# Optimization experiments

Measured on AMD Instinct MI355X. Metric: run time of the kernel, lower is better.

Reference implementation:

```python
import jax, jax.numpy as jnp
import numpy as np

B, P, EPG = 1000, 100, 1200  # graphs, nodes/graph, edges/graph
IN, HID, OUT, K = 16, 64, 5, 3


def setup_inputs() -> dict:
    key = jax.random.key(0)
    ks = jax.random.split(key, 12)
    offs = jnp.repeat(jnp.arange(B, dtype=jnp.int32) * P, EPG)
    src = jax.random.randint(ks[0], (B * EPG,), 0, P, dtype=jnp.int32) + offs
    dst = jax.random.randint(ks[1], (B * EPG,), 0, P, dtype=jnp.int32) + offs
    graph_ids = jnp.repeat(jnp.arange(B, dtype=jnp.int32), P)
    feat = jax.random.normal(ks[2], (B * P, IN), dtype=jnp.float32)

    def lin(k1, fan_in, fan_out):
        s = 1.0 / np.sqrt(fan_in)
        return jax.random.uniform(k1, (fan_in, fan_out), jnp.float32, -s, s)

    return {
        'feat': feat, 'src': src, 'dst': dst, 'graph_ids': graph_ids,
        'n_graphs': B,
        'W1': lin(ks[3], K * IN, HID), 'b1': jnp.zeros((HID,), jnp.float32),
        'W2': lin(ks[4], K * HID, HID), 'b2': jnp.zeros((HID,), jnp.float32),
        'W3': lin(ks[5], K * HID, HID), 'b3': jnp.zeros((HID,), jnp.float32),
        'Wfc': lin(ks[6], HID, OUT), 'bfc': jnp.zeros((OUT,), jnp.float32),
    }


def _cheb_conv(x, src, dst, d_invsqrt, W, b, k):
    # DGL ChebConv with lambda_max=2 -> re_norm=1, scaled Laplacian = -D^-1/2 A D^-1/2
    n = x.shape[0]

    def Ax(h):
        msg = (h * d_invsqrt)[src]                      # gather from source nodes
        agg = jax.ops.segment_sum(msg, dst, num_segments=n)
        return agg * d_invsqrt

    Xs = [x]
    if k > 1:
        Xs.append(-Ax(Xs[0]))                           # X1 = L_hat X0
        for _ in range(2, k):
            Xs.append(-2.0 * Ax(Xs[-1]) - Xs[-2])       # X_i = 2 L_hat X_{i-1} - X_{i-2}
    Xt = jnp.concatenate(Xs, axis=1)                    # [n, k*f]
    return Xt @ W + b


def reference(feat, src, dst, graph_ids, n_graphs, W1, b1, W2, b2, W3, b3, Wfc, bfc):
    n = feat.shape[0]
    deg = jax.ops.segment_sum(jnp.ones((src.shape[0],), feat.dtype), dst, num_segments=n)
    d_invsqrt = jnp.where(deg < 1.0, 1.0, deg) ** -0.5
    d_invsqrt = d_invsqrt[:, None]

    h = jax.nn.relu(_cheb_conv(feat, src, dst, d_invsqrt, W1, b1, K))
    h = jax.nn.relu(_cheb_conv(h, src, dst, d_invsqrt, W2, b2, K))
    h = jax.nn.relu(_cheb_conv(h, src, dst, d_invsqrt, W3, b3, K))

    # dgl.mean_nodes: per-graph mean pooling
    counts = jax.ops.segment_sum(jnp.ones((n,), h.dtype), graph_ids, num_segments=n_graphs)
    hg = jax.ops.segment_sum(h, graph_ids, num_segments=n_graphs) / counts[:, None]
    return hg @ Wfc + bfc
```

## Files before the change

kernel.cpp:

```cpp
#include <hip/hip_runtime.h>

#define NGRAPH 1000
#define P      100
#define EPG    1200
#define INF    16
#define HID    64
#define NOUT   5


#define ASTR   100
#define DINVC  64
#define DEGC   65
#define T1OFF  68
#define T2OFF  84

#define AINT_K   128
#define AINT_SZ  (P * AINT_K)

#define RK1    64
#define RK2    208
#define L1HI   0
#define L1LO   4096
#define L2HI   8192
#define L2LO   21504
#define L3HI   34816
#define L3LO   48128
#define WT_SHORTS 61440

typedef short short8 __attribute__((ext_vector_type(8)));
typedef float f32x4  __attribute__((ext_vector_type(4)));

__device__ __forceinline__ void bsplit(float x, short& h, short& l) {
    unsigned u = __float_as_uint(x);
    h = (short)(u >> 16);
    float hf = __uint_as_float(u & 0xffff0000u);
    l = (short)(__float_as_uint(x - hf) >> 16);
}

__global__ __launch_bounds__(256) void wprep(
    const float* __restrict__ W1, const float* __restrict__ W2,
    const float* __restrict__ W3, short* __restrict__ wt)
{
    const int i0 = blockIdx.x * blockDim.x + threadIdx.x;
    const int stride = gridDim.x * blockDim.x;
    for (int e = i0; e < HID * RK1; e += stride) {
        int c = e / RK1, r = e % RK1;
        float v = (r < 3 * INF) ? W1[r * HID + c] : 0.f;
        short h, l; bsplit(v, h, l);
        wt[L1HI + e] = h;
        wt[L1LO + e] = l;
    }
    for (int e = i0; e < HID * RK2; e += stride) {
        int c = e / RK2, r = e % RK2;
        float v2 = (r < 3 * HID) ? W2[r * HID + c] : 0.f;
        float v3 = (r < 3 * HID) ? W3[r * HID + c] : 0.f;
        short h, l;
        bsplit(v2, h, l); wt[L2HI + e] = h; wt[L2LO + e] = l;
        bsplit(v3, h, l); wt[L3HI + e] = h; wt[L3LO + e] = l;
    }
}

__global__ __launch_bounds__(256) void abuild(
    const int* __restrict__ src, const int* __restrict__ dst,
    short* __restrict__ aint)
{
    __shared__ unsigned int cnt[AINT_SZ / 2];
    const int g = blockIdx.x, tid = threadIdx.x, base = g * P;
    for (int i = tid; i < AINT_SZ / 2; i += 256) cnt[i] = 0u;
    __syncthreads();
    const int* srcg = src + g * EPG;
    const int* dstg = dst + g * EPG;
    for (int e = tid; e < EPG; e += 256) {
        int s = srcg[e] - base;
        int d = dstg[e] - base;
        int idx = d * AINT_K + s;
        atomicAdd(&cnt[idx >> 1], 1u << ((idx & 1) * 16));
    }
    __syncthreads();
    unsigned int* outw = (unsigned int*)(aint + (size_t)g * AINT_SZ);
    for (int i = tid; i < AINT_SZ / 2; i += 256) {
        unsigned int u = cnt[i];
        unsigned int b0 = __float_as_uint((float)(u & 0xffffu)) >> 16;
        unsigned int b1 = __float_as_uint((float)(u >> 16)) >> 16;
        outw[i] = b0 | (b1 << 16);
    }
}

template <int SECOND>
__device__ __forceinline__ void dense_prop(
    float* __restrict__ A, const short* __restrict__ aintg,
    int arow0, int arow1, bool has2,
    int srcoff, int dstoff, int ycol,
    int rb0, int rb1, f32x4 dv0, f32x4 dv1, int lane)
{
    const int n16 = lane & 15;
    const int q   = lane >> 4;
    const int kq  = q * 8;
    f32x4 p0, p1;
    p0[0]=0.f; p0[1]=0.f; p0[2]=0.f; p0[3]=0.f;
    p1[0]=0.f; p1[1]=0.f; p1[2]=0.f; p1[3]=0.f;
#pragma unroll
    for (int k = 0; k < 4; k++) {
        const short8 a0 = *(const short8*)&aintg[arow0 * AINT_K + k * 32 + kq];
        const short8 a1 = *(const short8*)&aintg[arow1 * AINT_K + k * 32 + kq];
        short8 bhi, blo; short h, l;
#pragma unroll
        for (int j = 0; j < 8; j++) {
            int row = k * 32 + kq + j;
            if (k == 3) row = (row < P) ? row : 0;
            float x = A[row * ASTR + srcoff + n16];
            bsplit(x, h, l); bhi[j] = h; blo[j] = l;
        }
        p0 = __builtin_amdgcn_mfma_f32_16x16x32_bf16(a0, bhi, p0, 0, 0, 0);
        p0 = __builtin_amdgcn_mfma_f32_16x16x32_bf16(a0, blo, p0, 0, 0, 0);
        if (has2) {
            p1 = __builtin_amdgcn_mfma_f32_16x16x32_bf16(a1, bhi, p1, 0, 0, 0);
            p1 = __builtin_amdgcn_mfma_f32_16x16x32_bf16(a1, blo, p1, 0, 0, 0);
        }
    }
#pragma unroll
    for (int r = 0; r < 4; r++) {
        const int row = rb0 + q * 4 + r;
        const float d2 = dv0[r] * dv0[r];
        float o;
        if (SECOND) o = -2.f * d2 * p0[r] - A[row * ASTR + ycol];
        else        o = -d2 * p0[r];
        A[row * ASTR + dstoff + n16] = o;
    }
    if (has2) {
#pragma unroll
        for (int r = 0; r < 4; r++) {
            const int row = rb1 + q * 4 + r;
            if (rb1 != 84 || row >= 96) {
                const float d2 = dv1[r] * dv1[r];
                float o;
                if (SECOND) o = -2.f * d2 * p1[r] - A[row * ASTR + ycol];
                else        o = -d2 * p1[r];
                A[row * ASTR + dstoff + n16] = o;
            }
        }
    }
}

template <int F, int FINAL>
__device__ __forceinline__ void cheb_layer(
    float* __restrict__ A, const short* __restrict__ aintg,
    const short* __restrict__ whi, const short* __restrict__ wlo,
    const float* __restrict__ bias,
    int tid, int rb0, int rb1, bool has2, f32x4 dv0, f32x4 dv1)
{
    const int RK   = 3 * F + 16;
    const int lane = tid & 63;
    const int wv   = tid >> 6;
    const int n16  = lane & 15;
    const int q    = lane >> 4;
    const int ncol = (wv << 4) + n16;

    const int arow0 = rb0 + n16;
    const int arow1 = (has2 ? rb1 : rb0) + n16;

    f32x4 acc[7];
#pragma unroll
    for (int t = 0; t < 7; t++) { acc[t][0]=0.f; acc[t][1]=0.f; acc[t][2]=0.f; acc[t][3]=0.f; }

    for (int cb = 0; cb < F; cb += 16) {
        dense_prop<0>(A, aintg, arow0, arow1, has2, cb, T1OFF, cb + n16,
                      rb0, rb1, dv0, dv1, lane);
        __syncthreads();
        dense_prop<1>(A, aintg, arow0, arow1, has2, T1OFF, T2OFF, cb + n16,
                      rb0, rb1, dv0, dv1, lane);
        __syncthreads();

#pragma unroll
        for (int ks = 0; ks < 2; ks++) {
            int wr, aoff;
            if (ks == 0) {
                wr   = (q == 0) ? cb : (q == 1) ? cb + 8 : (q == 2) ? F + cb : F + cb + 8;
                aoff = (q == 0) ? cb : (q == 1) ? cb + 8 : (q == 2) ? T1OFF  : T1OFF + 8;
            } else {
                wr   = (q == 0) ? 2*F + cb : (q == 1) ? 2*F + cb + 8 : (q == 2) ? 3*F : 3*F + 8;
                aoff = (q == 0) ? T2OFF    : (q == 1) ? T2OFF + 8    : (q == 2) ? T1OFF : T1OFF + 8;
            }
            const short8 bhi = *(const short8*)&whi[ncol * RK + wr];
            const short8 blo = *(const short8*)&wlo[ncol * RK + wr];
#pragma unroll
            for (int t = 0; t < 7; t++) {
                const int row = ((t < 6) ? t * 16 : 84) + n16;
                const float* xp = &A[row * ASTR + aoff];
                const float4 v0 = *(const float4*)xp;
                const float4 v1 = *(const float4*)(xp + 4);
                short8 ahi, alo; short h, l;
                bsplit(v0.x, h, l); ahi[0] = h; alo[0] = l;
                bsplit(v0.y, h, l); ahi[1] = h; alo[1] = l;
                bsplit(v0.z, h, l); ahi[2] = h; alo[2] = l;
                bsplit(v0.w, h, l); ahi[3] = h; alo[3] = l;
                bsplit(v1.x, h, l); ahi[4] = h; alo[4] = l;
                bsplit(v1.y, h, l); ahi[5] = h; alo[5] = l;
                bsplit(v1.z, h, l); ahi[6] = h; alo[6] = l;
                bsplit(v1.w, h, l); ahi[7] = h; alo[7] = l;
                acc[t] = __builtin_amdgcn_mfma_f32_16x16x32_bf16(ahi, bhi, acc[t], 0, 0, 0);
                acc[t] = __builtin_amdgcn_mfma_f32_16x16x32_bf16(ahi, blo, acc[t], 0, 0, 0);
                acc[t] = __builtin_amdgcn_mfma_f32_16x16x32_bf16(alo, bhi, acc[t], 0, 0, 0);
            }
        }
        __syncthreads();
    }

    const float bcol = bias[ncol];
#pragma unroll
    for (int t = 0; t < 7; t++) {
        const int rbase = ((t < 6) ? t * 16 : 84) + q * 4;
#pragma unroll
        for (int r = 0; r < 4; r++) {
            const int row = rbase + r;
            if (t < 6 || row >= 96) {
                const float dn = A[row * ASTR + DINVC];
                const float v = acc[t][r];
                float o;
                if (FINAL) o = fmaxf(v * (1.0f / dn) + bcol, 0.f);
                else       o = fmaxf(v + bcol * dn, 0.f);
                A[row * ASTR + ncol] = o;
            }
        }
    }
    __syncthreads();
}

__global__ __launch_bounds__(256, 4) void gnn_kernel(
    const float* __restrict__ feat,
    const int* __restrict__ src, const int* __restrict__ dst,
    const float* __restrict__ b1, const float* __restrict__ b2,
    const float* __restrict__ b3,
    const float* __restrict__ Wfc, const float* __restrict__ bfc,
    const short* __restrict__ wt, const short* __restrict__ aint,
    float* __restrict__ out)
{
    __shared__ __align__(16) float A[P * ASTR];
    const int g = blockIdx.x;
    const int tid = threadIdx.x;
    const int base = g * P;
    const int* dstg = dst + g * EPG;

    for (int i = tid; i < P; i += 256) *(int*)&A[i * ASTR + DEGC] = 0;
    __syncthreads();
    for (int e = tid; e < EPG; e += 256) {
        int d = dstg[e] - base;
        atomicAdd((int*)&A[d * ASTR + DEGC], 1);
    }
    __syncthreads();
    for (int i = tid; i < P; i += 256) {
        int dg = *(int*)&A[i * ASTR + DEGC];
        A[i * ASTR + DINVC] = rsqrtf((float)(dg > 1 ? dg : 1));
    }
    __syncthreads();

    for (int i = tid; i < P * INF / 4; i += 256) {
        int n = i >> 2, fq = (i & 3) * 4;
        float4 v = *(const float4*)&feat[(size_t)base * INF + i * 4];
        float dn = A[n * ASTR + DINVC];
        v.x *= dn; v.y *= dn; v.z *= dn; v.w *= dn;
        *(float4*)&A[n * ASTR + fq] = v;
    }
    __syncthreads();

    const int lane = tid & 63, wv = tid >> 6, q = lane >> 4;
    const int rb0 = wv * 16;
    const int t2i = wv + 4;
    const int rb1 = (t2i >= 6) ? 84 : t2i * 16;
    const bool has2 = (wv < 3);
    f32x4 dv0, dv1;
#pragma unroll
    for (int r = 0; r < 4; r++) {
        dv0[r] = A[(rb0 + q * 4 + r) * ASTR + DINVC];
        dv1[r] = A[((has2 ? rb1 : rb0) + q * 4 + r) * ASTR + DINVC];
    }

    const short* aintg = aint + (size_t)g * AINT_SZ;
    cheb_layer<INF, 0>(A, aintg, wt + L1HI, wt + L1LO, b1, tid, rb0, rb1, has2, dv0, dv1);
    cheb_layer<HID, 0>(A, aintg, wt + L2HI, wt + L2LO, b2, tid, rb0, rb1, has2, dv0, dv1);
    cheb_layer<HID, 1>(A, aintg, wt + L3HI, wt + L3LO, b3, tid, rb0, rb1, has2, dv0, dv1);

    {
        const int l2 = tid & 63, w = tid >> 6;
        float s = 0.f;
        for (int n = w; n < P; n += 4) s += A[n * ASTR + l2];
        A[l2 * ASTR + T1OFF + w] = s;
    }
    __syncthreads();
    if (tid < HID) {
        float hg = (A[tid * ASTR + T1OFF] + A[tid * ASTR + T1OFF + 1] +
                    A[tid * ASTR + T1OFF + 2] + A[tid * ASTR + T1OFF + 3]) * (1.0f / P);
        A[tid * ASTR + T1OFF + 4] = hg;
    }
    __syncthreads();
    if (tid < NOUT) {
        float o = bfc[tid];
        for (int c = 0; c < HID; c++) o += A[c * ASTR + T1OFF + 4] * Wfc[c * NOUT + tid];
        out[g * NOUT + tid] = o;
    }
}

extern "C" void kernel_launch(void* const* d_in, const int* in_sizes, int n_in,
                              void* d_out, int out_size, void* d_ws, size_t ws_size,
                              hipStream_t stream)
{
    const float* feat = (const float*)d_in[0];
    const int*   src  = (const int*)d_in[1];
    const int*   dst  = (const int*)d_in[2];
    const float* W1  = (const float*)d_in[5];
    const float* b1  = (const float*)d_in[6];
    const float* W2  = (const float*)d_in[7];
    const float* b2  = (const float*)d_in[8];
    const float* W3  = (const float*)d_in[9];
    const float* b3  = (const float*)d_in[10];
    const float* Wfc = (const float*)d_in[11];
    const float* bfc = (const float*)d_in[12];
    float* out = (float*)d_out;

    short* wt   = (short*)d_ws;
    short* aint = wt + WT_SHORTS;

    wprep<<<64, 256, 0, stream>>>(W1, W2, W3, wt);
    abuild<<<NGRAPH, 256, 0, stream>>>(src, dst, aint);
    gnn_kernel<<<NGRAPH, 256, 0, stream>>>(feat, src, dst,
                                           b1, b2, b3, Wfc, bfc, wt, aint, out);
}
```

Before: 161.7 us.

## Store shared activations as packed bf16 hi/lo pairs with swizzled layout

Shared-memory activations are now stored pre-split as packed bf16 hi/lo words, so MFMA operands are built with byte-permute instructions instead of repeating the float-to-bf16x2 split on every read. The shared tile gets an XOR swizzle on columns to reduce bank conflicts, and the adjacency MFMA fragments are loaded once into registers and reused across all three layers. The final pooling and FC use wave shuffles instead of extra shared-memory passes. This trades register pressure (held adjacency fragments) and a packing step at every store for cheaper inner loops. The rounding of the split changes slightly.

```diff
diff --git a/kernel.cpp b/kernel.cpp
--- a/kernel.cpp
+++ b/kernel.cpp
@@ -9,32 +9,61 @@
 
 
 #define ASTR   100
-#define DINVC  64
-#define DEGC   65
-#define T1OFF  68
-#define T2OFF  84
-
-#define AINT_K   128
-#define AINT_SZ  (P * AINT_K)
-
-#define RK1    64
-#define RK2    208
-#define L1HI   0
-#define L1LO   4096
-#define L2HI   8192
-#define L2LO   21504
-#define L3HI   34816
-#define L3LO   48128
+#define T1OFF  64
+#define T2OFF  80
+
+#define AINT_K  128
+#define AINT_SZ (P * AINT_K)
+
+#define RK1 64
+#define RK2 208
+#define L1HI 0
+#define L1LO 4096
+#define L2HI 8192
+#define L2LO 21504
+#define L3HI 34816
+#define L3LO 48128
 #define WT_SHORTS 61440
 
 typedef short short8 __attribute__((ext_vector_type(8)));
 typedef float f32x4  __attribute__((ext_vector_type(4)));
-
-__device__ __forceinline__ void bsplit(float x, short& h, short& l) {
-    unsigned u = __float_as_uint(x);
-    h = (short)(u >> 16);
-    float hf = __uint_as_float(u & 0xffff0000u);
-    l = (short)(__float_as_uint(x - hf) >> 16);
+typedef int   int4v  __attribute__((ext_vector_type(4)));
+
+__device__ __forceinline__ int sw(int row, int col) {
+    return row * ASTR + (col ^ (((row >> 3) & 3) << 3));
+}
+
+__device__ __forceinline__ unsigned packsplit(float x) {
+    unsigned u  = __float_as_uint(x);
+    unsigned hi = (u + 0x7fffu + ((u >> 16) & 1u)) >> 16;
+    float r = x - __uint_as_float(hi << 16);
+    unsigned v  = __float_as_uint(r);
+    unsigned lo = (v + 0x7fffu + ((v >> 16) & 1u)) >> 16;
+    return (hi << 16) | (lo & 0xffffu);
+}
+
+__device__ __forceinline__ float unpack(unsigned p) {
+    return __uint_as_float(p & 0xffff0000u) + __uint_as_float(p << 16);
+}
+
+#define PSEL_HI 0x07060302u
+#define PSEL_LO 0x05040100u
+
+__device__ __forceinline__ short8 mk_hi(const unsigned* u) {
+    int4v h;
+    h[0] = (int)__builtin_amdgcn_perm(u[1], u[0], PSEL_HI);
+    h[1] = (int)__builtin_amdgcn_perm(u[3], u[2], PSEL_HI);
+    h[2] = (int)__builtin_amdgcn_perm(u[5], u[4], PSEL_HI);
+    h[3] = (int)__builtin_amdgcn_perm(u[7], u[6], PSEL_HI);
+    return __builtin_bit_cast(short8, h);
+}
+__device__ __forceinline__ short8 mk_lo(const unsigned* u) {
+    int4v h;
+    h[0] = (int)__builtin_amdgcn_perm(u[1], u[0], PSEL_LO);
+    h[1] = (int)__builtin_amdgcn_perm(u[3], u[2], PSEL_LO);
+    h[2] = (int)__builtin_amdgcn_perm(u[5], u[4], PSEL_LO);
+    h[3] = (int)__builtin_amdgcn_perm(u[7], u[6], PSEL_LO);
+    return __builtin_bit_cast(short8, h);
 }
 
 __global__ __launch_bounds__(256) void wprep(
@@ -46,17 +75,17 @@
     for (int e = i0; e < HID * RK1; e += stride) {
         int c = e / RK1, r = e % RK1;
         float v = (r < 3 * INF) ? W1[r * HID + c] : 0.f;
-        short h, l; bsplit(v, h, l);
-        wt[L1HI + e] = h;
-        wt[L1LO + e] = l;
+        unsigned p = packsplit(v);
+        wt[L1HI + e] = (short)(p >> 16);
+        wt[L1LO + e] = (short)(p & 0xffffu);
     }
     for (int e = i0; e < HID * RK2; e += stride) {
         int c = e / RK2, r = e % RK2;
         float v2 = (r < 3 * HID) ? W2[r * HID + c] : 0.f;
         float v3 = (r < 3 * HID) ? W3[r * HID + c] : 0.f;
-        short h, l;
-        bsplit(v2, h, l); wt[L2HI + e] = h; wt[L2LO + e] = l;
-        bsplit(v3, h, l); wt[L3HI + e] = h; wt[L3LO + e] = l;
+        unsigned p2 = packsplit(v2), p3 = packsplit(v3);
+        wt[L2HI + e] = (short)(p2 >> 16); wt[L2LO + e] = (short)(p2 & 0xffffu);
+        wt[L3HI + e] = (short)(p3 >> 16); wt[L3LO + e] = (short)(p3 & 0xffffu);
     }
 }
 
@@ -88,9 +117,8 @@
 
 template <int SECOND>
 __device__ __forceinline__ void dense_prop(
-    float* __restrict__ A, const short* __restrict__ aintg,
-    int arow0, int arow1, bool has2,
-    int srcoff, int dstoff, int ycol,
+    unsigned* __restrict__ Ap, const short8* a0k, const short8* a1k, bool has2,
+    int srcoff, int dstoff, int ycb,
     int rb0, int rb1, f32x4 dv0, f32x4 dv1, int lane)
 {
     const int n16 = lane & 15;
@@ -101,21 +129,20 @@
     p1[0]=0.f; p1[1]=0.f; p1[2]=0.f; p1[3]=0.f;
 #pragma unroll
     for (int k = 0; k < 4; k++) {
-        const short8 a0 = *(const short8*)&aintg[arow0 * AINT_K + k * 32 + kq];
-        const short8 a1 = *(const short8*)&aintg[arow1 * AINT_K + k * 32 + kq];
-        short8 bhi, blo; short h, l;
+        unsigned u[8];
 #pragma unroll
         for (int j = 0; j < 8; j++) {
             int row = k * 32 + kq + j;
             if (k == 3) row = (row < P) ? row : 0;
-            float x = A[row * ASTR + srcoff + n16];
-            bsplit(x, h, l); bhi[j] = h; blo[j] = l;
-        }
-        p0 = __builtin_amdgcn_mfma_f32_16x16x32_bf16(a0, bhi, p0, 0, 0, 0);
-        p0 = __builtin_amdgcn_mfma_f32_16x16x32_bf16(a0, blo, p0, 0, 0, 0);
+            u[j] = Ap[sw(row, srcoff + n16)];
+        }
+        const short8 bhi = mk_hi(u);
+        const short8 blo = mk_lo(u);
+        p0 = __builtin_amdgcn_mfma_f32_16x16x32_bf16(a0k[k], bhi, p0, 0, 0, 0);
+        p0 = __builtin_amdgcn_mfma_f32_16x16x32_bf16(a0k[k], blo, p0, 0, 0, 0);
         if (has2) {
-            p1 = __builtin_amdgcn_mfma_f32_16x16x32_bf16(a1, bhi, p1, 0, 0, 0);
-            p1 = __builtin_amdgcn_mfma_f32_16x16x32_bf16(a1, blo, p1, 0, 0, 0);
+            p1 = __builtin_amdgcn_mfma_f32_16x16x32_bf16(a1k[k], bhi, p1, 0, 0, 0);
+            p1 = __builtin_amdgcn_mfma_f32_16x16x32_bf16(a1k[k], blo, p1, 0, 0, 0);
         }
     }
 #pragma unroll
@@ -123,9 +150,9 @@
         const int row = rb0 + q * 4 + r;
         const float d2 = dv0[r] * dv0[r];
         float o;
-        if (SECOND) o = -2.f * d2 * p0[r] - A[row * ASTR + ycol];
+        if (SECOND) o = -2.f * d2 * p0[r] - unpack(Ap[sw(row, ycb + n16)]);
         else        o = -d2 * p0[r];
-        A[row * ASTR + dstoff + n16] = o;
+        Ap[sw(row, dstoff + n16)] = packsplit(o);
     }
     if (has2) {
 #pragma unroll
@@ -134,9 +161,9 @@
             if (rb1 != 84 || row >= 96) {
                 const float d2 = dv1[r] * dv1[r];
                 float o;
-                if (SECOND) o = -2.f * d2 * p1[r] - A[row * ASTR + ycol];
+                if (SECOND) o = -2.f * d2 * p1[r] - unpack(Ap[sw(row, ycb + n16)]);
                 else        o = -d2 * p1[r];
-                A[row * ASTR + dstoff + n16] = o;
+                Ap[sw(row, dstoff + n16)] = packsplit(o);
             }
         }
     }
@@ -144,10 +171,11 @@
 
 template <int F, int FINAL>
 __device__ __forceinline__ void cheb_layer(
-    float* __restrict__ A, const short* __restrict__ aintg,
+    unsigned* __restrict__ Ap, const float* __restrict__ dinv,
+    const short8* a0k, const short8* a1k, bool has2,
     const short* __restrict__ whi, const short* __restrict__ wlo,
     const float* __restrict__ bias,
-    int tid, int rb0, int rb1, bool has2, f32x4 dv0, f32x4 dv1)
+    int tid, int rb0, int rb1, f32x4 dv0, f32x4 dv1)
 {
     const int RK   = 3 * F + 16;
     const int lane = tid & 63;
@@ -156,19 +184,14 @@
     const int q    = lane >> 4;
     const int ncol = (wv << 4) + n16;
 
-    const int arow0 = rb0 + n16;
-    const int arow1 = (has2 ? rb1 : rb0) + n16;
-
     f32x4 acc[7];
 #pragma unroll
     for (int t = 0; t < 7; t++) { acc[t][0]=0.f; acc[t][1]=0.f; acc[t][2]=0.f; acc[t][3]=0.f; }
 
     for (int cb = 0; cb < F; cb += 16) {
-        dense_prop<0>(A, aintg, arow0, arow1, has2, cb, T1OFF, cb + n16,
-                      rb0, rb1, dv0, dv1, lane);
+        dense_prop<0>(Ap, a0k, a1k, has2, cb,    T1OFF, 0,  rb0, rb1, dv0, dv1, lane);
         __syncthreads();
-        dense_prop<1>(A, aintg, arow0, arow1, has2, T1OFF, T2OFF, cb + n16,
-                      rb0, rb1, dv0, dv1, lane);
+        dense_prop<1>(Ap, a0k, a1k, has2, T1OFF, T2OFF, cb, rb0, rb1, dv0, dv1, lane);
         __syncthreads();
 
 #pragma unroll
@@ -186,18 +209,14 @@
 #pragma unroll
             for (int t = 0; t < 7; t++) {
                 const int row = ((t < 6) ? t * 16 : 84) + n16;
-                const float* xp = &A[row * ASTR + aoff];
-                const float4 v0 = *(const float4*)xp;
-                const float4 v1 = *(const float4*)(xp + 4);
-                short8 ahi, alo; short h, l;
-                bsplit(v0.x, h, l); ahi[0] = h; alo[0] = l;
-                bsplit(v0.y, h, l); ahi[1] = h; alo[1] = l;
-                bsplit(v0.z, h, l); ahi[2] = h; alo[2] = l;
-                bsplit(v0.w, h, l); ahi[3] = h; alo[3] = l;
-                bsplit(v1.x, h, l); ahi[4] = h; alo[4] = l;
-                bsplit(v1.y, h, l); ahi[5] = h; alo[5] = l;
-                bsplit(v1.z, h, l); ahi[6] = h; alo[6] = l;
-                bsplit(v1.w, h, l); ahi[7] = h; alo[7] = l;
+                const unsigned* xp = &Ap[sw(row, aoff)];
+                const int4v w0 = *(const int4v*)xp;
+                const int4v w1 = *(const int4v*)(xp + 4);
+                unsigned u[8];
+                u[0]=(unsigned)w0[0]; u[1]=(unsigned)w0[1]; u[2]=(unsigned)w0[2]; u[3]=(unsigned)w0[3];
+                u[4]=(unsigned)w1[0]; u[5]=(unsigned)w1[1]; u[6]=(unsigned)w1[2]; u[7]=(unsigned)w1[3];
+                const short8 ahi = mk_hi(u);
+                const short8 alo = mk_lo(u);
                 acc[t] = __builtin_amdgcn_mfma_f32_16x16x32_bf16(ahi, bhi, acc[t], 0, 0, 0);
                 acc[t] = __builtin_amdgcn_mfma_f32_16x16x32_bf16(ahi, blo, acc[t], 0, 0, 0);
                 acc[t] = __builtin_amdgcn_mfma_f32_16x16x32_bf16(alo, bhi, acc[t], 0, 0, 0);
@@ -214,12 +233,12 @@
         for (int r = 0; r < 4; r++) {
             const int row = rbase + r;
             if (t < 6 || row >= 96) {
-                const float dn = A[row * ASTR + DINVC];
+                const float dn = dinv[row];
                 const float v = acc[t][r];
                 float o;
                 if (FINAL) o = fmaxf(v * (1.0f / dn) + bcol, 0.f);
                 else       o = fmaxf(v + bcol * dn, 0.f);
-                A[row * ASTR + ncol] = o;
+                Ap[sw(row, ncol)] = packsplit(o);
             }
         }
     }
@@ -235,35 +254,39 @@
     const short* __restrict__ wt, const short* __restrict__ aint,
     float* __restrict__ out)
 {
-    __shared__ __align__(16) float A[P * ASTR];
+    __shared__ __align__(16) unsigned Ap[P * ASTR];
+    __shared__ float meta[128];
+
     const int g = blockIdx.x;
     const int tid = threadIdx.x;
     const int base = g * P;
     const int* dstg = dst + g * EPG;
 
-    for (int i = tid; i < P; i += 256) *(int*)&A[i * ASTR + DEGC] = 0;
-    __syncthreads();
-    for (int e = tid; e < EPG; e += 256) {
-        int d = dstg[e] - base;
-        atomicAdd((int*)&A[d * ASTR + DEGC], 1);
-    }
+    int* deg = (int*)meta;
+    for (int i = tid; i < P; i += 256) deg[i] = 0;
+    __syncthreads();
+    for (int e = tid; e < EPG; e += 256) atomicAdd(&deg[dstg[e] - base], 1);
     __syncthreads();
     for (int i = tid; i < P; i += 256) {
-        int dg = *(int*)&A[i * ASTR + DEGC];
-        A[i * ASTR + DINVC] = rsqrtf((float)(dg > 1 ? dg : 1));
+        int dg = deg[i];
+        meta[i] = rsqrtf((float)(dg > 1 ? dg : 1));
     }
     __syncthreads();
 
     for (int i = tid; i < P * INF / 4; i += 256) {
-        int n = i >> 2, fq = (i & 3) * 4;
+        int n = i >> 2, f0 = (i & 3) * 4;
         float4 v = *(const float4*)&feat[(size_t)base * INF + i * 4];
-        float dn = A[n * ASTR + DINVC];
-        v.x *= dn; v.y *= dn; v.z *= dn; v.w *= dn;
-        *(float4*)&A[n * ASTR + fq] = v;
-    }
-    __syncthreads();
-
-    const int lane = tid & 63, wv = tid >> 6, q = lane >> 4;
+        float dn = meta[n];
+        int4v pk;
+        pk[0] = (int)packsplit(v.x * dn);
+        pk[1] = (int)packsplit(v.y * dn);
+        pk[2] = (int)packsplit(v.z * dn);
+        pk[3] = (int)packsplit(v.w * dn);
+        *(int4v*)&Ap[sw(n, f0)] = pk;
+    }
+    __syncthreads();
+
+    const int lane = tid & 63, wv = tid >> 6, q = lane >> 4, n16 = lane & 15;
     const int rb0 = wv * 16;
     const int t2i = wv + 4;
     const int rb1 = (t2i >= 6) ? 84 : t2i * 16;
@@ -271,32 +294,52 @@
     f32x4 dv0, dv1;
 #pragma unroll
     for (int r = 0; r < 4; r++) {
-        dv0[r] = A[(rb0 + q * 4 + r) * ASTR + DINVC];
-        dv1[r] = A[((has2 ? rb1 : rb0) + q * 4 + r) * ASTR + DINVC];
-    }
-
+        dv0[r] = meta[rb0 + q * 4 + r];
+        dv1[r] = meta[(has2 ? rb1 : rb0) + q * 4 + r];
+    }
     const short* aintg = aint + (size_t)g * AINT_SZ;
-    cheb_layer<INF, 0>(A, aintg, wt + L1HI, wt + L1LO, b1, tid, rb0, rb1, has2, dv0, dv1);
-    cheb_layer<HID, 0>(A, aintg, wt + L2HI, wt + L2LO, b2, tid, rb0, rb1, has2, dv0, dv1);
-    cheb_layer<HID, 1>(A, aintg, wt + L3HI, wt + L3LO, b3, tid, rb0, rb1, has2, dv0, dv1);
+    const int arow0 = rb0 + n16;
+    const int arow1 = (has2 ? rb1 : rb0) + n16;
+    short8 a0k[4], a1k[4];
+#pragma unroll
+    for (int k = 0; k < 4; k++) {
+        a0k[k] = *(const short8*)&aintg[arow0 * AINT_K + k * 32 + q * 8];
+        a1k[k] = *(const short8*)&aintg[arow1 * AINT_K + k * 32 + q * 8];
+    }
+
+    cheb_layer<INF, 0>(Ap, meta, a0k, a1k, has2, wt + L1HI, wt + L1LO, b1, tid, rb0, rb1, dv0, dv1);
+    cheb_layer<HID, 0>(Ap, meta, a0k, a1k, has2, wt + L2HI, wt + L2LO, b2, tid, rb0, rb1, dv0, dv1);
+    cheb_layer<HID, 1>(Ap, meta, a0k, a1k, has2, wt + L3HI, wt + L3LO, b3, tid, rb0, rb1, dv0, dv1);
 
     {
-        const int l2 = tid & 63, w = tid >> 6;
+        const int l = tid & 63, w = tid >> 6;
         float s = 0.f;
-        for (int n = w; n < P; n += 4) s += A[n * ASTR + l2];
-        A[l2 * ASTR + T1OFF + w] = s;
-    }
-    __syncthreads();
-    if (tid < HID) {
-        float hg = (A[tid * ASTR + T1OFF] + A[tid * ASTR + T1OFF + 1] +
-                    A[tid * ASTR + T1OFF + 2] + A[tid * ASTR + T1OFF + 3]) * (1.0f / P);
-        A[tid * ASTR + T1OFF + 4] = hg;
+        for (int n = w; n < P; n += 4) s += unpack(Ap[sw(n, l)]);
+        float o0 = s * Wfc[l * NOUT + 0];
+        float o1 = s * Wfc[l * NOUT + 1];
+        float o2 = s * Wfc[l * NOUT + 2];
+        float o3 = s * Wfc[l * NOUT + 3];
+        float o4 = s * Wfc[l * NOUT + 4];
+#pragma unroll
+        for (int d = 1; d < 64; d <<= 1) {
+            o0 += __shfl_xor(o0, d);
+            o1 += __shfl_xor(o1, d);
+            o2 += __shfl_xor(o2, d);
+            o3 += __shfl_xor(o3, d);
+            o4 += __shfl_xor(o4, d);
+        }
+        if (l == 0) {
+            meta[100 + w * NOUT + 0] = o0;
+            meta[100 + w * NOUT + 1] = o1;
+            meta[100 + w * NOUT + 2] = o2;
+            meta[100 + w * NOUT + 3] = o3;
+            meta[100 + w * NOUT + 4] = o4;
+        }
     }
     __syncthreads();
     if (tid < NOUT) {
-        float o = bfc[tid];
-        for (int c = 0; c < HID; c++) o += A[c * ASTR + T1OFF + 4] * Wfc[c * NOUT + tid];
-        out[g * NOUT + tid] = o;
+        float o = meta[100 + tid] + meta[105 + tid] + meta[110 + tid] + meta[115 + tid];
+        out[g * NOUT + tid] = bfc[tid] + o * (1.0f / P);
     }
 }
 
```

After: 186.0 us. 1.15x slower.
